# Kernel optimization log

Hardware: AMD Instinct MI355X
Metric: run time of the kernel (lower is better)

Reference implementation:

```python
import jax, jax.numpy as jnp
import numpy as np

MERGE_R = 2048


def setup_inputs() -> dict:
    key = jax.random.key(0)
    k1, k2 = jax.random.split(key, 2)
    B, N, C = 4, 8192, 512
    x = jax.random.normal(k1, (B, N, C), jnp.float32)
    W = jax.random.normal(k2, (C // 4, C), jnp.float32) * 0.02  # Linear(dim, dim//4)
    b = jnp.zeros((C // 4,), jnp.float32)
    return {"x": x, "W": W, "b": b}


def reference(x, W, b):
    B, N, C = x.shape
    r = min(MERGE_R, N // 2)

    # metric projection; matching is done under no_grad in the original
    metric = jax.lax.stop_gradient(x @ W.T + b)
    metric = metric / jnp.linalg.norm(metric, axis=-1, keepdims=True)

    a = metric[:, 0::2]   # [B, N/2, C/4] evens
    bt = metric[:, 1::2]  # [B, N/2, C/4] odds
    scores = jnp.einsum('bad,bcd->bac', a, bt)  # [B, N/2, N/2]
    values = scores.max(axis=-1)                # [B, N/2] best score per even token
    node_indices = scores.argmax(axis=-1)       # [B, N/2] best odd partner per even
    _, top_b_indices = jax.lax.top_k(values, r) # [B, r]

    bidx = jnp.arange(B)[:, None]
    global_b = top_b_indices * 2 + 1                                  # [B, r] odd positions removed
    matched_a = jnp.take_along_axis(node_indices, top_b_indices, 1)   # [B, r]
    global_a = matched_a * 2                                          # [B, r] even positions merged into

    # boolean keep-mask: exactly r False per row (topk indices are distinct)
    mask = jnp.ones((B, N), bool).at[bidx, global_b].set(False)

    b_feat = jnp.take_along_axis(x, global_b[:, :, None], axis=1)     # [B, r, C]
    x_out = x.at[bidx, global_a].add(b_feat)                          # scatter-add merge
    counts = jnp.ones((B, N, 1), x.dtype).at[bidx, global_a].add(1.0)
    x_out = x_out / counts

    # compact kept rows: stable argsort of ~mask keeps original order of True entries
    kept = jnp.argsort(~mask, axis=1)[:, : N - r]                     # [B, N-r]
    x_final = jnp.take_along_axis(x_out, kept[:, :, None], axis=1)    # [B, N-r, C]

    # ownership / unmerge map
    new_idx = jnp.cumsum(mask.astype(jnp.int32), axis=1) - 1          # [B, N]
    ownership = jnp.where(mask, new_idx, 0)
    target_a_new = jnp.take_along_axis(new_idx, global_a, axis=1)
    ownership = ownership.at[bidx, global_b].set(target_a_new)
    return x_final, ownership
```

## Files before the change

### kernel.cpp

```cpp
#include <hip/hip_runtime.h>
#include <cstdint>
#include <cstddef>

#define BQ    4
#define NTOK  8192
#define CDIM  512
#define MDIM  128
#define NA    4096
#define RSEL  2048
#define NKEEP (NTOK - RSEL)
#define RESCUE_CAP 2048
#define GAP_DELTA 2e-4f
#define WIN_TAU   2e-4f
#define CSPL  16

typedef float f32x4 __attribute__((ext_vector_type(4)));
typedef short short8 __attribute__((ext_vector_type(8)));

static __device__ __forceinline__ unsigned short bf16rne(float f) {
  unsigned u = __float_as_uint(f);
  return (unsigned short)((u + 0x7FFFu + ((u >> 16) & 1)) >> 16);
}

__device__ __forceinline__ unsigned long long rank_select_4096(
    const unsigned long long* keysL, unsigned* histL,
    unsigned long long* candL, unsigned* scanL, unsigned* shw ,
    int rank, int t) {
  unsigned long long pval = 0ull, pmask = 0ull;
  int curRank = rank;
  for (int lvl = 0; lvl < 3; ++lvl) {
    const int shift = 52 - lvl * 12;
#pragma unroll
    for (int i = 0; i < 4; ++i) histL[t + i * 1024] = 0;
    __syncthreads();
#pragma unroll
    for (int i = 0; i < 4; ++i) {
      unsigned long long k = keysL[t + i * 1024];
      if ((k & pmask) == pval)
        atomicAdd(&histL[(unsigned)((k >> shift) & 0xFFFull)], 1u);
    }
    __syncthreads();
    unsigned s = histL[4 * t] + histL[4 * t + 1] + histL[4 * t + 2] + histL[4 * t + 3];
    scanL[t] = s;
    __syncthreads();
    for (int off = 1; off < 1024; off <<= 1) {
      unsigned v = (t >= off) ? scanL[t - off] : 0;
      __syncthreads();
      scanL[t] += v;
      __syncthreads();
    }
    const unsigned incl = scanL[t], excl = incl - s;
    if ((int)excl <= curRank && curRank < (int)incl) {
      int r = curRank - (int)excl;
      unsigned b = 4 * t;
#pragma unroll
      for (int q = 0; q < 4; ++q) {
        unsigned c = histL[4 * t + q];
        if (r < (int)c) { b = 4 * t + q; break; }
        r -= (int)c;
      }
      shw[0] = b; shw[1] = (unsigned)r; shw[3] = histL[b];
    }
    __syncthreads();
    const unsigned bucket = shw[0];
    curRank = (int)shw[1];
    const unsigned cntB = shw[3];
    pval |= ((unsigned long long)bucket) << shift;
    pmask |= 0xFFFull << shift;
    if (cntB <= 1024u) break;
  }
  if (t == 0) shw[2] = 0;
  __syncthreads();
#pragma unroll
  for (int i = 0; i < 4; ++i) {
    unsigned long long k = keysL[t + i * 1024];
    if ((k & pmask) == pval) {
      unsigned pos = atomicAdd(&shw[2], 1u);
      if (pos < 1024u) candL[pos] = k;
    }
  }
  __syncthreads();
  const int c1 = (int)shw[2];
  int P = 64;
  while (P < c1) P <<= 1;
  for (int p = t; p < P; p += 1024)
    if (p >= c1) candL[p] = ~0ull;
  __syncthreads();
  for (int k2 = 2; k2 <= P; k2 <<= 1)
    for (int j = k2 >> 1; j > 0; j >>= 1) {
      for (int p = t; p < P; p += 1024) {
        int q = p ^ j;
        if (q > p) {
          bool up = ((p & k2) == 0);
          unsigned long long a = candL[p], c = candL[q];
          if ((a > c) == up) { candL[p] = c; candL[q] = a; }
        }
      }
      __syncthreads();
    }
  return candL[curRank];
}

__global__ __launch_bounds__(128) void k_metric(const float* __restrict__ X,
                                                const float* __restrict__ W,
                                                const float* __restrict__ bias,
                                                float* __restrict__ ma,
                                                float* __restrict__ mb,
                                                unsigned short* __restrict__ maH,
                                                unsigned short* __restrict__ maM,
                                                unsigned short* __restrict__ mbH,
                                                unsigned short* __restrict__ mbM) {
  __shared__ float ldsA[2][64 * 32];
  __shared__ float ldsB[2][128 * 32];
  __shared__ float snorm[64 * 16];
  __shared__ float sinv[64];
  const int t = threadIdx.x;
  const int tok0 = blockIdx.x * 64;
  const int r8 = t & 7, cg = t >> 3;

  float acc[8][8];
#pragma unroll
  for (int i = 0; i < 8; ++i)
#pragma unroll
    for (int j = 0; j < 8; ++j) acc[i][j] = 0.f;

  const char* aSrc[4];
  const char* bSrc[8];
#pragma unroll
  for (int i = 0; i < 4; ++i) {
    int s = i * 128 + t, row = s >> 3, gr = s & 7;
    aSrc[i] = (const char*)(X + (size_t)(tok0 + row) * CDIM) + ((gr ^ (row & 7)) << 4);
  }
#pragma unroll
  for (int i = 0; i < 8; ++i) {
    int s = i * 128 + t, row = s >> 3, gr = s & 7;
    bSrc[i] = (const char*)(W + (size_t)row * CDIM) + ((gr ^ ((row >> 3) & 7)) << 4);
  }

  auto stage = [&](int bufn, int kc) {
    const size_t off = (size_t)kc << 7;
    char* da = (char*)&ldsA[bufn][0] + t * 16;
    char* db = (char*)&ldsB[bufn][0] + t * 16;
#pragma unroll
    for (int i = 0; i < 4; ++i)
      __builtin_amdgcn_global_load_lds(
          (const __attribute__((address_space(1))) void*)(aSrc[i] + off),
          (__attribute__((address_space(3))) void*)(da + i * 2048), 16, 0, 0);
#pragma unroll
    for (int i = 0; i < 8; ++i)
      __builtin_amdgcn_global_load_lds(
          (const __attribute__((address_space(1))) void*)(bSrc[i] + off),
          (__attribute__((address_space(3))) void*)(db + i * 2048), 16, 0, 0);
  };

  auto compute = [&](int bufn) {
#pragma unroll
    for (int kq = 0; kq < 8; ++kq) {
      const int gA = (kq ^ r8) << 2;
      const int gB = (kq ^ (cg & 7)) << 2;
      float4 av[8], bv[8];
#pragma unroll
      for (int i = 0; i < 8; ++i)
        av[i] = *(const float4*)&ldsA[bufn][(r8 + (i << 3)) * 32 + gA];
#pragma unroll
      for (int j = 0; j < 8; ++j)
        bv[j] = *(const float4*)&ldsB[bufn][((cg << 3) + j) * 32 + gB];
#pragma unroll
      for (int i = 0; i < 8; ++i)
#pragma unroll
        for (int j = 0; j < 8; ++j) {
          acc[i][j] = fmaf(av[i].x, bv[j].x, acc[i][j]);
          acc[i][j] = fmaf(av[i].y, bv[j].y, acc[i][j]);
          acc[i][j] = fmaf(av[i].z, bv[j].z, acc[i][j]);
          acc[i][j] = fmaf(av[i].w, bv[j].w, acc[i][j]);
        }
    }
  };

  stage(0, 0);
  __syncthreads();
  for (int kc = 0; kc < 16; ++kc) {
    if (kc + 1 < 16) stage((kc + 1) & 1, kc + 1);
    compute(kc & 1);
    __syncthreads();
  }

  float bb[8];
#pragma unroll
  for (int j = 0; j < 8; ++j) bb[j] = bias[(cg << 3) + j];
#pragma unroll
  for (int i = 0; i < 8; ++i) {
    float s = 0.f;
#pragma unroll
    for (int j = 0; j < 8; ++j) {
      acc[i][j] += bb[j];
      s = fmaf(acc[i][j], acc[i][j], s);
    }
    snorm[(r8 + (i << 3)) * 16 + cg] = s;
  }
  __syncthreads();
  if (t < 64) {
    float s = 0.f;
    for (int q = 0; q < 16; ++q) s += snorm[t * 16 + q];
    sinv[t] = 1.0f / sqrtf(s);
  }
  __syncthreads();
#pragma unroll
  for (int i = 0; i < 8; ++i) {
    int r = r8 + (i << 3);
    int tokg = tok0 + r;
    float inv = sinv[r];
    int bq = tokg >> 13, pos = tokg & (NTOK - 1);
    size_t eidx = ((size_t)bq * NA + (pos >> 1)) * MDIM + (cg << 3);
    float vv[8];
#pragma unroll
    for (int j = 0; j < 8; ++j) vv[j] = acc[i][j] * inv;
    float* dst = ((pos & 1) ? mb : ma) + eidx;
    *(float4*)dst = make_float4(vv[0], vv[1], vv[2], vv[3]);
    *(float4*)(dst + 4) = make_float4(vv[4], vv[5], vv[6], vv[7]);
    unsigned hB[8], mB[8];
#pragma unroll
    for (int j = 0; j < 8; ++j) {
      hB[j] = bf16rne(vv[j]);
      mB[j] = bf16rne(vv[j] - __uint_as_float(hB[j] << 16));
    }
    uint4 hw, mw;
    hw.x = hB[0] | (hB[1] << 16); hw.y = hB[2] | (hB[3] << 16);
    hw.z = hB[4] | (hB[5] << 16); hw.w = hB[6] | (hB[7] << 16);
    mw.x = mB[0] | (mB[1] << 16); mw.y = mB[2] | (mB[3] << 16);
    mw.z = mB[4] | (mB[5] << 16); mw.w = mB[6] | (mB[7] << 16);
    *(uint4*)(((pos & 1) ? mbH : maH) + eidx) = hw;
    *(uint4*)(((pos & 1) ? mbM : maM) + eidx) = mw;
  }
}

__global__ __launch_bounds__(256, 3) void k_scores_mfma(
    const unsigned short* __restrict__ maH, const unsigned short* __restrict__ maM,
    const unsigned short* __restrict__ mbH, const unsigned short* __restrict__ mbM,
    float* __restrict__ pv1, int* __restrict__ pi1, float* __restrict__ pv2) {
  __shared__ short8 lds8[2][2][16][16];
  const int t = threadIdx.x;
  const int bid = blockIdx.x;
  const int bq = bid >> 9, rem = bid & 511, at = rem >> 4, cs = rem & 15;
  const int a0 = at * 128;
  const int l = t & 63, w = t >> 6;
  const int l15 = l & 15, l4 = l >> 4;

  short8 aH[2][4], aM[2][4];
#pragma unroll
  for (int rf = 0; rf < 2; ++rf)
#pragma unroll
    for (int kc = 0; kc < 4; ++kc) {
      size_t aidx = ((size_t)bq * NA + a0 + w * 32 + rf * 16 + l15) * MDIM
                    + kc * 32 + l4 * 8;
      aH[rf][kc] = *(const short8*)(maH + aidx);
      aM[rf][kc] = *(const short8*)(maM + aidx);
    }

  const int scl = t >> 4, sg = t & 15;
  const size_t srow = ((size_t)bq * NA + cs * 256 + scl) << 8;
  const size_t soff = srow + (size_t)((sg ^ (scl & 7)) << 4);
  const char* spH = (const char*)mbH + soff;
  const char* spM = (const char*)mbM + soff;

  auto stage = [&](int bufn) {
    char* dst = (char*)&lds8[bufn][0][0][0] + t * 16;
    __builtin_amdgcn_global_load_lds(
        (const __attribute__((address_space(1))) void*)spH,
        (__attribute__((address_space(3))) void*)dst, 16, 0, 0);
    __builtin_amdgcn_global_load_lds(
        (const __attribute__((address_space(1))) void*)spM,
        (__attribute__((address_space(3))) void*)(dst + 4096), 16, 0, 0);
    spH += 4096; spM += 4096;
  };

  float bv1[8], bv2[8];
  int bi1[8];
#pragma unroll
  for (int s = 0; s < 8; ++s) { bv1[s] = -1e30f; bv2[s] = -1e30f; bi1[s] = 0x7FFFFFFF; }

  auto compute = [&](int bufn, int cbase) {
    f32x4 acc1[2], acc2[2];
    acc1[0] = 0.f; acc1[1] = 0.f; acc2[0] = 0.f; acc2[1] = 0.f;
#pragma unroll
    for (int kc = 0; kc < 4; ++kc) {
      const int gg = (kc * 4 + l4) ^ (l15 & 7);
      short8 bh = lds8[bufn][0][l15][gg];
      short8 bm = lds8[bufn][1][l15][gg];
#pragma unroll
      for (int rf = 0; rf < 2; ++rf) {
        acc1[rf] = __builtin_amdgcn_mfma_f32_16x16x32_bf16(aH[rf][kc], bh, acc1[rf], 0, 0, 0);
        acc2[rf] = __builtin_amdgcn_mfma_f32_16x16x32_bf16(aH[rf][kc], bm, acc2[rf], 0, 0, 0);
        acc2[rf] = __builtin_amdgcn_mfma_f32_16x16x32_bf16(aM[rf][kc], bh, acc2[rf], 0, 0, 0);
      }
    }
    const int cg = cbase + l15;
#pragma unroll
    for (int rf = 0; rf < 2; ++rf) {
      f32x4 v4 = acc1[rf] + acc2[rf];
#pragma unroll
      for (int r2 = 0; r2 < 4; ++r2) {
        float v = v4[r2];
        int s = rf * 4 + r2;
        if (v > bv1[s]) { bv2[s] = bv1[s]; bv1[s] = v; bi1[s] = cg; }
        else if (v > bv2[s]) bv2[s] = v;
      }
    }
  };

  stage(0);
  __syncthreads();
  const int cb0 = cs * 256;
  for (int chp = 0; chp < 8; ++chp) {
    const int ch = chp * 2;
    if (ch + 1 < 16) stage(1);
    compute(0, cb0 + ch * 16);
    __syncthreads();
    if (ch + 2 < 16) stage(0);
    compute(1, cb0 + ch * 16 + 16);
    __syncthreads();
  }

#pragma unroll
  for (int s = 0; s < 8; ++s) {
    float v1 = bv1[s], v2 = bv2[s];
    int i1 = bi1[s];
#pragma unroll
    for (int m = 1; m < 16; m <<= 1) {
      float V1 = __shfl_xor(v1, m);
      int I1 = __shfl_xor(i1, m);
      float V2 = __shfl_xor(v2, m);
      bool take = (V1 > v1) || (V1 == v1 && I1 < i1);
      float lose = take ? v1 : V1;
      if (take) { v1 = V1; i1 = I1; }
      v2 = fmaxf(fmaxf(v2, V2), lose);
    }
    if (l15 == s) {
      int row = a0 + w * 32 + (s >> 2) * 16 + (l4 << 2) + (s & 3);
      size_t off = ((size_t)(bq * CSPL + cs)) * NA + row;
      pv1[off] = v1; pi1[off] = i1; pv2[off] = v2;
    }
  }
}

__global__ __launch_bounds__(1024) void k_mergemark(
    const float* __restrict__ pv1, const int* __restrict__ pi1,
    const float* __restrict__ pv2,
    float* __restrict__ valA, int* __restrict__ nodeA,
    int* __restrict__ rescueCnt, int* __restrict__ rescueIdx,
    int* __restrict__ cnt, int* __restrict__ head,
    unsigned long long* __restrict__ rescueKey) {
  __shared__ unsigned long long keys[NA];
  __shared__ unsigned hist[NA];
  __shared__ unsigned long long cand[1024];
  __shared__ unsigned scan1[1024];
  __shared__ unsigned shw[4];
  const int b = blockIdx.x, t = threadIdx.x;
  if (t == 0) rescueCnt[b] = 0;
  float gval[4], ggap[4];
#pragma unroll
  for (int k4 = 0; k4 < 4; ++k4) {
    const int p = t + k4 * 1024;
    const size_t i = (size_t)b * NA + p;
    float v1 = -1e30f, v2 = -1e30f;
    int i1 = 0x7FFFFFFF;
#pragma unroll
    for (int cspl = 0; cspl < CSPL; ++cspl) {
      size_t o = ((size_t)(b * CSPL + cspl)) * NA + p;
      float V1 = pv1[o], V2 = pv2[o];
      int I1 = pi1[o];
      bool take = (V1 > v1) || (V1 == v1 && I1 < i1);
      float lose = take ? v1 : V1;
      if (take) { v1 = V1; i1 = I1; }
      v2 = fmaxf(fmaxf(v2, V2), lose);
    }
    valA[i] = v1; nodeA[i] = i1;
    cnt[i] = 0; head[i] = -1; rescueKey[i] = 0ull;
    gval[k4] = v1; ggap[k4] = v1 - v2;
    unsigned u = __float_as_uint(v1);
    unsigned mono = u ^ ((u >> 31) ? 0xFFFFFFFFu : 0x80000000u);
    keys[p] = ((unsigned long long)(~mono) << 32) | (unsigned)p;
  }
  __syncthreads();

  const unsigned long long thr =
      rank_select_4096(keys, hist, cand, scan1, shw, RSEL - 1, t);
  unsigned monoT = ~(unsigned)(thr >> 32);
  unsigned uT = (monoT >> 31) ? (monoT ^ 0x80000000u) : ~monoT;
  const float vb = __uint_as_float(uT);

#pragma unroll
  for (int k4 = 0; k4 < 4; ++k4) {
    const int p = t + k4 * 1024;
    if (ggap[k4] < GAP_DELTA || fabsf(gval[k4] - vb) <= WIN_TAU) {
      int slot = atomicAdd(&rescueCnt[b], 1);
      if (slot < RESCUE_CAP) rescueIdx[b * RESCUE_CAP + slot] = p;
    }
  }
}

__global__ __launch_bounds__(256) void k_rescue(const float* __restrict__ ma,
                                                const float* __restrict__ mb,
                                                const int* __restrict__ rescueIdx,
                                                const int* __restrict__ rescueCnt,
                                                unsigned long long* __restrict__ key) {
  const int bq = blockIdx.x >> 8;
  const int wid = blockIdx.x & 255;
  const int cnt = min(rescueCnt[bq], RESCUE_CAP);
  const int npair = cnt * 16;
  const int t = threadIdx.x;
  __shared__ float sA[128];
  __shared__ float wv[4];
  __shared__ int   wi[4];
  for (int pair = wid; pair < npair; pair += 256) {
    const int slot = pair >> 4, chunk = pair & 15;
    const int row = rescueIdx[bq * RESCUE_CAP + slot];
    __syncthreads();
    if (t < 128) sA[t] = ma[((size_t)bq * NA + row) * MDIM + t];
    __syncthreads();
    const int c = chunk * 256 + t;
    const float* bp = mb + ((size_t)bq * NA + c) * MDIM;
    float d0 = 0.f, d1 = 0.f, d2 = 0.f, d3 = 0.f;
#pragma unroll
    for (int j = 0; j < 8; ++j) {
      float4 b0 = *(const float4*)(bp + j * 16 + 0);
      float4 b1 = *(const float4*)(bp + j * 16 + 4);
      float4 b2 = *(const float4*)(bp + j * 16 + 8);
      float4 b3 = *(const float4*)(bp + j * 16 + 12);
      const float4 a0 = *(const float4*)&sA[j * 16 + 0];
      const float4 a1 = *(const float4*)&sA[j * 16 + 4];
      const float4 a2 = *(const float4*)&sA[j * 16 + 8];
      const float4 a3 = *(const float4*)&sA[j * 16 + 12];
      d0 = fmaf(a0.x, b0.x, d0); d0 = fmaf(a0.y, b0.y, d0);
      d0 = fmaf(a0.z, b0.z, d0); d0 = fmaf(a0.w, b0.w, d0);
      d1 = fmaf(a1.x, b1.x, d1); d1 = fmaf(a1.y, b1.y, d1);
      d1 = fmaf(a1.z, b1.z, d1); d1 = fmaf(a1.w, b1.w, d1);
      d2 = fmaf(a2.x, b2.x, d2); d2 = fmaf(a2.y, b2.y, d2);
      d2 = fmaf(a2.z, b2.z, d2); d2 = fmaf(a2.w, b2.w, d2);
      d3 = fmaf(a3.x, b3.x, d3); d3 = fmaf(a3.y, b3.y, d3);
      d3 = fmaf(a3.z, b3.z, d3); d3 = fmaf(a3.w, b3.w, d3);
    }
    float d = (d0 + d1) + (d2 + d3);
    int ci = c;
#pragma unroll
    for (int m = 1; m < 64; m <<= 1) {
      float V = __shfl_xor(d, m);
      int C = __shfl_xor(ci, m);
      if (V > d || (V == d && C < ci)) { d = V; ci = C; }
    }
    if ((t & 63) == 0) { wv[t >> 6] = d; wi[t >> 6] = ci; }
    __syncthreads();
    if (t == 0) {
      for (int w2 = 1; w2 < 4; ++w2)
        if (wv[w2] > d || (wv[w2] == d && wi[w2] < ci)) { d = wv[w2]; ci = wi[w2]; }
      unsigned u = __float_as_uint(d);
      unsigned mono = u ^ ((u >> 31) ? 0xFFFFFFFFu : 0x80000000u);
      unsigned long long k = ((unsigned long long)mono << 32)
                           | (unsigned)(0xFFFFFFFFu - (unsigned)ci);
      atomicMax(&key[(size_t)bq * NA + row], k);
    }
  }
}

__global__ __launch_bounds__(1024) void k_select(
    const unsigned long long* __restrict__ rescueKey,
    const float* __restrict__ valA, const int* __restrict__ nodeA,
    int* __restrict__ sel, int* __restrict__ cnt, int* __restrict__ head,
    int* __restrict__ nxt, int* __restrict__ newidx,
    float* __restrict__ own) {
  __shared__ unsigned long long keys[NA];
  __shared__ int nodeL[NA];
  __shared__ unsigned char selL[NA];
  __shared__ int ni[NTOK];
  __shared__ unsigned tot[1024];
  __shared__ unsigned hist[NA];
  __shared__ unsigned long long cand[1024];
  __shared__ unsigned shw[4];
  const int b = blockIdx.x, t = threadIdx.x;

#pragma unroll
  for (int k4 = 0; k4 < 4; ++k4) {
    const int p = t + k4 * 1024;
    const size_t i = (size_t)b * NA + p;
    unsigned long long rk = rescueKey[i];
    float v; int nd;
    if (rk) {
      unsigned mono = (unsigned)(rk >> 32);
      unsigned u = (mono & 0x80000000u) ? (mono ^ 0x80000000u) : ~mono;
      v = __uint_as_float(u);
      nd = (int)(0xFFFFFFFFu - (unsigned)(rk & 0xFFFFFFFFull));
    } else {
      v = valA[i];
      nd = nodeA[i];
    }
    nodeL[p] = nd;
    unsigned u = __float_as_uint(v);
    unsigned mono = u ^ ((u >> 31) ? 0xFFFFFFFFu : 0x80000000u);
    keys[p] = ((unsigned long long)(~mono) << 32) | (unsigned)p;
  }
  __syncthreads();

  const unsigned long long thr =
      rank_select_4096(keys, hist, cand, tot, shw, RSEL - 1, t);

#pragma unroll
  for (int k4 = 0; k4 < 4; ++k4) {
    const int p = t + k4 * 1024;
    selL[p] = (keys[p] <= thr) ? 1 : 0;
  }
  __syncthreads();

#pragma unroll
  for (int k4 = 0; k4 < 4; ++k4) {
    const int p = t + k4 * 1024;
    const size_t i = (size_t)b * NA + p;
    int s = selL[p];
    sel[i] = s;
    if (s) {
      int dst = nodeL[p];
      atomicAdd(&cnt[(size_t)b * NA + dst], 1);
      nxt[i] = atomicExch(&head[(size_t)b * NA + dst], p);
    }
  }

  const int base = t * 8;
  int kept[8], run = 0;
#pragma unroll
  for (int e = 0; e < 8; ++e) {
    int idx = base + e;
    int kp = ((idx & 1) == 0) ? 1 : (selL[idx >> 1] ? 0 : 1);
    kept[e] = kp;
    run += kp;
  }
  tot[t] = (unsigned)run;
  __syncthreads();
  for (int off = 1; off < 1024; off <<= 1) {
    unsigned v = (t >= off) ? tot[t - off] : 0;
    __syncthreads();
    tot[t] += v;
    __syncthreads();
  }
  int cum = (int)tot[t] - run;
#pragma unroll
  for (int e = 0; e < 8; ++e) {
    cum += kept[e];
    ni[base + e] = cum - 1;
  }
  __syncthreads();
#pragma unroll
  for (int e = 0; e < 8; ++e) {
    int idx = base + e;
    int ow = kept[e] ? ni[idx] : ni[2 * nodeL[idx >> 1]];
    newidx[(size_t)b * NTOK + idx] = ni[idx];
    own[(size_t)b * NTOK + idx] = (float)ow;
  }
}

__global__ __launch_bounds__(256) void k_assemble(const float* __restrict__ X,
                                                  const int* __restrict__ sel,
                                                  const int* __restrict__ newidx,
                                                  const int* __restrict__ cnt,
                                                  const int* __restrict__ head,
                                                  const int* __restrict__ nxt,
                                                  float* __restrict__ out) {
  const int token = blockIdx.x * 2 + (threadIdx.x >> 7);
  const int bq = token >> 13, tp = token & (NTOK - 1);
  const int t = threadIdx.x & 127;
  if ((tp & 1) && sel[(size_t)bq * NA + (tp >> 1)]) return;
  float4 v = *(const float4*)(X + (size_t)token * CDIM + t * 4);
  if (!(tp & 1)) {
    size_t slot = (size_t)bq * NA + (tp >> 1);
    int c = cnt[slot];
    if (c > 0) {
      int kk = head[slot];
      while (kk >= 0) {
        float4 s = *(const float4*)(X + ((size_t)bq * NTOK + 2 * kk + 1) * CDIM + t * 4);
        v.x += s.x; v.y += s.y; v.z += s.z; v.w += s.w;
        kk = nxt[(size_t)bq * NA + kk];
      }
      float inv = 1.0f / (float)(1 + c);
      v.x *= inv; v.y *= inv; v.z *= inv; v.w *= inv;
    }
  }
  int dst = newidx[(size_t)bq * NTOK + tp];
  *(float4*)(out + ((size_t)bq * NKEEP + dst) * CDIM + t * 4) = v;
}

extern "C" void kernel_launch(void* const* d_in, const int* in_sizes, int n_in,
                              void* d_out, int out_size, void* d_ws, size_t ws_size,
                              hipStream_t stream) {
  const float* X    = (const float*)d_in[0];
  const float* W    = (const float*)d_in[1];
  const float* bias = (const float*)d_in[2];
  float* out = (float*)d_out;
  char* ws = (char*)d_ws;

  size_t o = 0;
  float* ma   = (float*)(ws + o); o += (size_t)BQ * NA * MDIM * 4;
  float* mb   = (float*)(ws + o); o += (size_t)BQ * NA * MDIM * 4;
  unsigned short* maH = (unsigned short*)(ws + o); o += (size_t)BQ * NA * MDIM * 2;
  unsigned short* maM = (unsigned short*)(ws + o); o += (size_t)BQ * NA * MDIM * 2;
  unsigned short* mbH = (unsigned short*)(ws + o); o += (size_t)BQ * NA * MDIM * 2;
  unsigned short* mbM = (unsigned short*)(ws + o); o += (size_t)BQ * NA * MDIM * 2;
  float* pv1  = (float*)(ws + o); o += (size_t)BQ * CSPL * NA * 4;
  int*   pi1  = (int*)(ws + o);   o += (size_t)BQ * CSPL * NA * 4;
  float* pv2  = (float*)(ws + o); o += (size_t)BQ * CSPL * NA * 4;
  float* valA = (float*)(ws + o); o += (size_t)BQ * NA * 4;
  int*   nodeA= (int*)(ws + o);   o += (size_t)BQ * NA * 4;
  int*   sel  = (int*)(ws + o);   o += (size_t)BQ * NA * 4;
  int*   cnt  = (int*)(ws + o);   o += (size_t)BQ * NA * 4;
  int*   head = (int*)(ws + o);   o += (size_t)BQ * NA * 4;
  int*   nxt  = (int*)(ws + o);   o += (size_t)BQ * NA * 4;
  int*   newidx = (int*)(ws + o); o += (size_t)BQ * NTOK * 4;
  int*   rescueCnt = (int*)(ws + o); o += 256;
  int*   rescueIdx = (int*)(ws + o); o += (size_t)BQ * RESCUE_CAP * 4;
  unsigned long long* rescueKey = (unsigned long long*)(ws + o); o += (size_t)BQ * NA * 8;
  (void)in_sizes; (void)n_in; (void)out_size; (void)ws_size;

  k_metric<<<512, 128, 0, stream>>>(X, W, bias, ma, mb, maH, maM, mbH, mbM);
  k_scores_mfma<<<BQ * 32 * CSPL, 256, 0, stream>>>(maH, maM, mbH, mbM, pv1, pi1, pv2);
  k_mergemark<<<BQ, 1024, 0, stream>>>(pv1, pi1, pv2, valA, nodeA,
                                       rescueCnt, rescueIdx, cnt, head, rescueKey);
  k_rescue<<<BQ * 256, 256, 0, stream>>>(ma, mb, rescueIdx, rescueCnt, rescueKey);
  k_select<<<BQ, 1024, 0, stream>>>(rescueKey, valA, nodeA, sel, cnt, head, nxt,
                                    newidx, out + (size_t)BQ * NKEEP * CDIM);
  k_assemble<<<BQ * NTOK / 2, 256, 0, stream>>>(X, sel, newidx, cnt, head, nxt, out);
}
```

Baseline: 316.4 us.

## Give each wave private LDS staging buffers and drop block-wide barriers in score kernel

The score kernel now gives each wave its own double-buffered LDS tile, which it fills and consumes itself. This replaces __syncthreads with per-wave s_waitcnt vmcnt waits so waves no longer stall on each other. The column split is halved, so each block walks 512 odd tokens in 32 chunks, and launch bounds drop to 2 blocks per CU. The trade-off is 4x more LDS and redundant B-tile loads per wave, in exchange for fewer barriers, fewer blocks and fewer partial results to merge downstream.

```diff
diff --git a/kernel.cpp b/kernel.cpp
--- a/kernel.cpp
+++ b/kernel.cpp
@@ -12,7 +12,7 @@
 #define RESCUE_CAP 2048
 #define GAP_DELTA 2e-4f
 #define WIN_TAU   2e-4f
-#define CSPL  16
+#define CSPL  8
 
 typedef float f32x4 __attribute__((ext_vector_type(4)));
 typedef short short8 __attribute__((ext_vector_type(8)));
@@ -234,14 +234,14 @@
   }
 }
 
-__global__ __launch_bounds__(256, 3) void k_scores_mfma(
+__global__ __launch_bounds__(256, 2) void k_scores_mfma(
     const unsigned short* __restrict__ maH, const unsigned short* __restrict__ maM,
     const unsigned short* __restrict__ mbH, const unsigned short* __restrict__ mbM,
     float* __restrict__ pv1, int* __restrict__ pi1, float* __restrict__ pv2) {
-  __shared__ short8 lds8[2][2][16][16];
+  __shared__ short8 lds8[4][2][2][16][16];
   const int t = threadIdx.x;
   const int bid = blockIdx.x;
-  const int bq = bid >> 9, rem = bid & 511, at = rem >> 4, cs = rem & 15;
+  const int bq = bid >> 8, rem = bid & 255, at = rem >> 3, cs = rem & 7;
   const int a0 = at * 128;
   const int l = t & 63, w = t >> 6;
   const int l15 = l & 15, l4 = l >> 4;
@@ -257,21 +257,25 @@
       aM[rf][kc] = *(const short8*)(maM + aidx);
     }
 
-  const int scl = t >> 4, sg = t & 15;
-  const size_t srow = ((size_t)bq * NA + cs * 256 + scl) << 8;
-  const size_t soff = srow + (size_t)((sg ^ (scl & 7)) << 4);
-  const char* spH = (const char*)mbH + soff;
-  const char* spM = (const char*)mbM + soff;
+  const char* sp[8];
+#pragma unroll
+  for (int i = 0; i < 8; ++i) {
+    const int ci = (i & 3) * 4 + (l >> 4);
+    const int gi = l & 15;
+    const char* base = (const char*)((i >> 2) ? mbM : mbH);
+    sp[i] = base + (((size_t)bq * NA + cs * 512 + ci) << 8)
+                 + ((gi ^ (ci & 7)) << 4);
+  }
 
   auto stage = [&](int bufn) {
-    char* dst = (char*)&lds8[bufn][0][0][0] + t * 16;
-    __builtin_amdgcn_global_load_lds(
-        (const __attribute__((address_space(1))) void*)spH,
-        (__attribute__((address_space(3))) void*)dst, 16, 0, 0);
-    __builtin_amdgcn_global_load_lds(
-        (const __attribute__((address_space(1))) void*)spM,
-        (__attribute__((address_space(3))) void*)(dst + 4096), 16, 0, 0);
-    spH += 4096; spM += 4096;
+    char* dst = (char*)&lds8[w][bufn][0][0][0] + l * 16;
+#pragma unroll
+    for (int i = 0; i < 8; ++i) {
+      __builtin_amdgcn_global_load_lds(
+          (const __attribute__((address_space(1))) void*)sp[i],
+          (__attribute__((address_space(3))) void*)(dst + i * 1024), 16, 0, 0);
+      sp[i] += 4096;
+    }
   };
 
   float bv1[8], bv2[8];
@@ -285,8 +289,8 @@
 #pragma unroll
     for (int kc = 0; kc < 4; ++kc) {
       const int gg = (kc * 4 + l4) ^ (l15 & 7);
-      short8 bh = lds8[bufn][0][l15][gg];
-      short8 bm = lds8[bufn][1][l15][gg];
+      short8 bh = lds8[w][bufn][0][l15][gg];
+      short8 bm = lds8[w][bufn][1][l15][gg];
 #pragma unroll
       for (int rf = 0; rf < 2; ++rf) {
         acc1[rf] = __builtin_amdgcn_mfma_f32_16x16x32_bf16(aH[rf][kc], bh, acc1[rf], 0, 0, 0);
@@ -308,17 +312,17 @@
     }
   };
 
+  asm volatile("s_waitcnt vmcnt(0)" ::: "memory");
   stage(0);
-  __syncthreads();
-  const int cb0 = cs * 256;
-  for (int chp = 0; chp < 8; ++chp) {
-    const int ch = chp * 2;
-    if (ch + 1 < 16) stage(1);
-    compute(0, cb0 + ch * 16);
-    __syncthreads();
-    if (ch + 2 < 16) stage(0);
-    compute(1, cb0 + ch * 16 + 16);
-    __syncthreads();
+  const int cb0 = cs * 512;
+  for (int ch = 0; ch < 32; ++ch) {
+    if (ch + 1 < 32) {
+      stage((ch + 1) & 1);
+      asm volatile("s_waitcnt vmcnt(8)" ::: "memory");
+    } else {
+      asm volatile("s_waitcnt vmcnt(0)" ::: "memory");
+    }
+    compute(ch & 1, cb0 + ch * 16);
   }
 
 #pragma unroll
@@ -618,7 +622,7 @@
   (void)in_sizes; (void)n_in; (void)out_size; (void)ws_size;
 
   k_metric<<<512, 128, 0, stream>>>(X, W, bias, ma, mb, maH, maM, mbH, mbM);
-  k_scores_mfma<<<BQ * 32 * CSPL, 256, 0, stream>>>(maH, maM, mbH, mbM, pv1, pi1, pv2);
+  k_scores_mfma<<<BQ * 32 * 8, 256, 0, stream>>>(maH, maM, mbH, mbM, pv1, pi1, pv2);
   k_mergemark<<<BQ, 1024, 0, stream>>>(pv1, pi1, pv2, valA, nodeA,
                                        rescueCnt, rescueIdx, cnt, head, rescueKey);
   k_rescue<<<BQ * 256, 256, 0, stream>>>(ma, mb, rescueIdx, rescueCnt, rescueKey);
```

New measurement: 292.2 us. 7.6% less time.
